# Kernel tuning notes

Measured on AMD Instinct MI355X. Metric: run time of the kernel, lower is better.

The kernel has to match this reference:

```python
import jax, jax.numpy as jnp
import numpy as np

B, S, H, I, E, K = 2, 2048, 1024, 2816, 8, 2


def setup_inputs() -> dict:
    key = jax.random.key(0)
    k1, k2, k3, k4, k5 = jax.random.split(key, 5)
    std = 0.02
    x = jax.random.normal(k1, (B, S, H), dtype=jnp.float32)
    gate_w = jax.random.normal(k2, (H, E), dtype=jnp.float32) * std   # router Linear(H,E), no bias
    Wg = jax.random.normal(k3, (E, H, I), dtype=jnp.float32) * std    # per-expert gate_proj
    Wu = jax.random.normal(k4, (E, H, I), dtype=jnp.float32) * std    # per-expert up_proj
    Wd = jax.random.normal(k5, (E, I, H), dtype=jnp.float32) * std    # per-expert down_proj
    return {"x": x, "gate_w": gate_w, "Wg": Wg, "Wu": Wu, "Wd": Wd}


def reference(x, gate_w, Wg, Wu, Wd):
    b, s, h = x.shape
    e = gate_w.shape[1]
    # --- Gating ---
    logits = jnp.einsum('bsh,he->bse', x, gate_w)                      # [B,S,E]
    top_vals, top_idx = jax.lax.top_k(logits, K)                       # [B,S,K]
    sel = (top_idx[..., None] == jnp.arange(e)).any(axis=-2)           # [B,S,E] bool, top-k mask
    sparse_logits = jnp.where(sel, logits, -jnp.inf)
    sparse_probs = jax.nn.softmax(sparse_logits, axis=-1)              # zero weight off top-k
    # --- Experts (dense over E, weighted by sparse probs; math identical to gather/scatter loop) ---
    xf = x.reshape(-1, h)                                              # [T,H], T=B*S
    g = jnp.einsum('th,ehi->tei', xf, Wg)                              # [T,E,I]
    u = jnp.einsum('th,ehi->tei', xf, Wu)
    act = jax.nn.silu(g) * u                                           # SwiGLU
    expert_out = jnp.einsum('tei,eih->teh', act, Wd)                   # [T,E,H]
    out = jnp.einsum('teh,te->th', expert_out, sparse_probs.reshape(-1, e))
    final_outputs = out.reshape(b, s, h)
    gate_logit = logits.reshape(-1, e)                                 # [B*S,E]
    return final_outputs, gate_logit
```

## Files before the change

kernel.cpp:

```cpp
#include <hip/hip_runtime.h>


namespace {
constexpr int TOKS = 4096;
constexpr int HDIM = 1024;
constexpr int IDIM = 2816;
constexpr int NEXP = 8;
constexpr int NROW = 8192;

constexpr size_t WGT_OFF = 0;
constexpr size_t WUT_OFF = 46137344;
constexpr size_t WDT_OFF = 92274688;
constexpr size_t A_OFF   = 138412032;
constexpr size_t ACT_OFF = 155189248;
constexpr size_t CNT_OFF = 201326592;
constexpr size_t OFS_OFF = CNT_OFF + 64;
constexpr size_t TLN_OFF = CNT_OFF + 128;
constexpr size_t TLS_OFF = CNT_OFF + 256;
constexpr size_t TIX_OFF = CNT_OFF + 1024;
constexpr size_t TPR_OFF = CNT_OFF + 66560;
constexpr size_t PRT_OFF = 0;
}

typedef __attribute__((ext_vector_type(8))) short short8;
typedef __attribute__((ext_vector_type(8))) unsigned short ushort8;
typedef __attribute__((ext_vector_type(4))) float f32x4;

__device__ __forceinline__ unsigned short f2bf(float f) {
  union { float f; unsigned int u; } v; v.f = f;
  unsigned int u = v.u;
  return (unsigned short)((u + 0x7fffu + ((u >> 16) & 1u)) >> 16);
}

__device__ __forceinline__ void gl2lds16(const void* g, void* l) {
  __builtin_amdgcn_global_load_lds(
      (const __attribute__((address_space(1))) void*)g,
      (__attribute__((address_space(3))) void*)l, 16, 0, 0);
}

__global__ __launch_bounds__(256) void k_transpose_all(
    const float* __restrict__ Wg, const float* __restrict__ Wu,
    const float* __restrict__ Wd, unsigned short* __restrict__ WgT,
    unsigned short* __restrict__ WuT, unsigned short* __restrict__ WdT,
    int* __restrict__ cnt) {
  const int z = blockIdx.z;
  if (z == 0 && blockIdx.x == 0 && threadIdx.x < NEXP) cnt[threadIdx.x] = 0;
  const float* in; unsigned short* out; int C, R;
  if (z < 8)       { in = Wg; out = WgT; C = IDIM; R = HDIM; }
  else if (z < 16) { in = Wu; out = WuT; C = IDIM; R = HDIM; }
  else             { in = Wd; out = WdT; C = HDIM; R = IDIM; }
  const size_t eoff = (size_t)(z & 7) * HDIM * IDIM;
  in += eoff; out += eoff;
  const int nbx = C / 64;
  const int c0 = (blockIdx.x % nbx) * 64, r0 = (blockIdx.x / nbx) * 64;
  __shared__ float tile[64][65];
  const int tid = threadIdx.x;
  const int rr = tid >> 4, cc4 = (tid & 15) * 4;
#pragma unroll
  for (int i = 0; i < 4; ++i) {
    int r = rr + i * 16;
    float4 v = *(const float4*)(in + (size_t)(r0 + r) * C + c0 + cc4);
    tile[r][cc4 + 0] = v.x; tile[r][cc4 + 1] = v.y;
    tile[r][cc4 + 2] = v.z; tile[r][cc4 + 3] = v.w;
  }
  __syncthreads();
  const int j = tid & 7;
#pragma unroll
  for (int i = 0; i < 2; ++i) {
    int c = (tid >> 3) + i * 32;
    ushort8 o;
#pragma unroll
    for (int k = 0; k < 8; ++k) o[k] = f2bf(tile[j * 8 + k][c]);
    *(ushort8*)(out + (size_t)(c0 + c) * R + r0 + j * 8) = o;
  }
}

__global__ __launch_bounds__(256) void k_gating(
    const float* __restrict__ x, const float* __restrict__ gw,
    float* __restrict__ logits_out, int* __restrict__ cnt,
    int4* __restrict__ tidx, float2* __restrict__ tprb) {
  const int lane = threadIdx.x & 63;
  const int t = blockIdx.x * 4 + (threadIdx.x >> 6);
  const float4* xr = (const float4*)(x + (size_t)t * HDIM);
  double acc[8];
#pragma unroll
  for (int e = 0; e < 8; ++e) acc[e] = 0.0;
#pragma unroll
  for (int jj = 0; jj < 4; ++jj) {
    float4 xv = xr[lane + jj * 64];
    const int hb = (lane + jj * 64) * 4;
    const float xs[4] = {xv.x, xv.y, xv.z, xv.w};
#pragma unroll
    for (int c = 0; c < 4; ++c) {
      const float4* g = (const float4*)(gw + (size_t)(hb + c) * 8);
      float4 g0 = g[0], g1 = g[1];
      acc[0] += (double)xs[c] * g0.x; acc[1] += (double)xs[c] * g0.y;
      acc[2] += (double)xs[c] * g0.z; acc[3] += (double)xs[c] * g0.w;
      acc[4] += (double)xs[c] * g1.x; acc[5] += (double)xs[c] * g1.y;
      acc[6] += (double)xs[c] * g1.z; acc[7] += (double)xs[c] * g1.w;
    }
  }
#pragma unroll
  for (int off = 32; off > 0; off >>= 1) {
#pragma unroll
    for (int e = 0; e < 8; ++e) acc[e] += __shfl_down(acc[e], off);
  }
  if (lane == 0) {
    float lg[8];
#pragma unroll
    for (int e = 0; e < 8; ++e) lg[e] = (float)acc[e];
#pragma unroll
    for (int e = 0; e < 8; ++e) logits_out[(size_t)t * 8 + e] = lg[e];
    float v0 = lg[0]; int i0 = 0; float v1 = -3.0e38f; int i1 = 0;
#pragma unroll
    for (int e = 1; e < 8; ++e) {
      if (lg[e] > v0) { v1 = v0; i1 = i0; v0 = lg[e]; i0 = e; }
      else if (lg[e] > v1) { v1 = lg[e]; i1 = e; }
    }
    float ex = expf(v1 - v0);
    float p0 = 1.0f / (1.0f + ex);
    float p1 = ex / (1.0f + ex);
    int r0 = atomicAdd(&cnt[i0], 1);
    int r1 = atomicAdd(&cnt[i1], 1);
    tidx[t] = make_int4(i0, i1, r0, r1);
    tprb[t] = make_float2(p0, p1);
  }
}

__global__ void k_prefix(const int* __restrict__ cnt, int* __restrict__ offs,
                         int2* __restrict__ tlist, int* __restrict__ tln) {
  if (threadIdx.x == 0) {
    int s = 0, nt = 0;
    for (int e = 0; e < NEXP; ++e) {
      offs[e] = s;
      for (int m0 = 0; m0 < cnt[e]; m0 += 128) tlist[nt++] = make_int2(e, m0);
      s += cnt[e];
    }
    *tln = nt;
  }
}

__global__ __launch_bounds__(256) void k_build(
    const float* __restrict__ x, const int4* __restrict__ tidx,
    const int* __restrict__ offs, unsigned short* __restrict__ A) {
  const int t = blockIdx.x;
  const int4 ii = tidx[t];
  const int r0 = offs[ii.x] + ii.z, r1 = offs[ii.y] + ii.w;
  float4 v = ((const float4*)(x + (size_t)t * HDIM))[threadIdx.x];
  ushort4 b;
  b.x = f2bf(v.x); b.y = f2bf(v.y); b.z = f2bf(v.z); b.w = f2bf(v.w);
  ((ushort4*)(A + (size_t)r0 * HDIM))[threadIdx.x] = b;
  ((ushort4*)(A + (size_t)r1 * HDIM))[threadIdx.x] = b;
}

__global__ __launch_bounds__(256, 2) void k_gemm1(
    const unsigned short* __restrict__ A, const unsigned short* __restrict__ WgT,
    const unsigned short* __restrict__ WuT, unsigned short* __restrict__ act,
    const int* __restrict__ cnt, const int* __restrict__ offs,
    const int2* __restrict__ tlist, const int* __restrict__ tln) {
  if ((int)blockIdx.y >= *tln) return;
  const int2 tl = tlist[blockIdx.y];
  const int e = tl.x, m0 = tl.y;
  const int ne = cnt[e];
  const int off = offs[e];
  const int n0 = blockIdx.x * 64;
  const unsigned short* Bg = WgT + ((size_t)e * IDIM + n0) * HDIM;
  const unsigned short* Bu = WuT + ((size_t)e * IDIM + n0) * HDIM;

  __shared__ unsigned short As[128 * 64];
  __shared__ unsigned short Bgs[64 * 64];
  __shared__ unsigned short Bus[64 * 64];

  const int tid = threadIdx.x, w = tid >> 6, lane = tid & 63;
  const int lrow8 = lane >> 3;
  const int swz = ((lane & 7) ^ lrow8) * 8;
  const int m16 = lane & 15, quad = lane >> 4, l7 = lane & 7;

  f32x4 accg[2][4], accu[2][4];
#pragma unroll
  for (int mi = 0; mi < 2; ++mi)
#pragma unroll
    for (int ni = 0; ni < 4; ++ni) {
      accg[mi][ni] = (f32x4){0.f, 0.f, 0.f, 0.f};
      accu[mi][ni] = (f32x4){0.f, 0.f, 0.f, 0.f};
    }

  for (int kt = 0; kt < HDIM / 64; ++kt) {
    const int k0 = kt * 64;
#pragma unroll
    for (int i = 0; i < 4; ++i) {
      int gr = off + m0 + w * 32 + i * 8 + lrow8;
      gr = gr > (NROW - 1) ? (NROW - 1) : gr;
      gl2lds16(A + (size_t)gr * HDIM + k0 + swz, &As[(w * 32 + i * 8) * 64]);
    }
#pragma unroll
    for (int i = 0; i < 2; ++i) {
      int rl = w * 16 + i * 8 + lrow8;
      gl2lds16(Bg + (size_t)rl * HDIM + k0 + swz, &Bgs[(w * 16 + i * 8) * 64]);
      gl2lds16(Bu + (size_t)rl * HDIM + k0 + swz, &Bus[(w * 16 + i * 8) * 64]);
    }
    __syncthreads();
#pragma unroll
    for (int kk = 0; kk < 2; ++kk) {
      const int jc = ((kk * 4 + quad) ^ l7) * 8;
      short8 af[2], bgf[4], buf[4];
#pragma unroll
      for (int mi = 0; mi < 2; ++mi)
        af[mi] = *(const short8*)&As[(w * 32 + mi * 16 + m16) * 64 + jc];
#pragma unroll
      for (int ni = 0; ni < 4; ++ni) {
        bgf[ni] = *(const short8*)&Bgs[(ni * 16 + m16) * 64 + jc];
        buf[ni] = *(const short8*)&Bus[(ni * 16 + m16) * 64 + jc];
      }
#pragma unroll
      for (int mi = 0; mi < 2; ++mi)
#pragma unroll
        for (int ni = 0; ni < 4; ++ni) {
          accg[mi][ni] = __builtin_amdgcn_mfma_f32_16x16x32_bf16(
              af[mi], bgf[ni], accg[mi][ni], 0, 0, 0);
          accu[mi][ni] = __builtin_amdgcn_mfma_f32_16x16x32_bf16(
              af[mi], buf[ni], accu[mi][ni], 0, 0, 0);
        }
    }
    __syncthreads();
  }
#pragma unroll
  for (int mi = 0; mi < 2; ++mi)
#pragma unroll
    for (int ni = 0; ni < 4; ++ni)
#pragma unroll
      for (int r = 0; r < 4; ++r) {
        int ml = w * 32 + mi * 16 + quad * 4 + r;
        float g = accg[mi][ni][r];
        float u = accu[mi][ni][r];
        float s = g / (1.0f + __expf(-g));
        As[ml * 64 + ni * 16 + m16] = f2bf(s * u);
      }
  __syncthreads();
#pragma unroll
  for (int i = 0; i < 4; ++i) {
    int chunk = i * 256 + tid;
    int row = chunk >> 3, j = chunk & 7;
    if (m0 + row < ne)
      *(ushort8*)&act[(size_t)(off + m0 + row) * IDIM + n0 + j * 8] =
          *(const ushort8*)&As[row * 64 + j * 8];
  }
}

__global__ __launch_bounds__(256, 2) void k_gemm2(
    const unsigned short* __restrict__ act, const unsigned short* __restrict__ WdT,
    float* __restrict__ partial, const int* __restrict__ cnt,
    const int* __restrict__ offs, const int2* __restrict__ tlist,
    const int* __restrict__ tln) {
  if ((int)blockIdx.y >= *tln) return;
  const int2 tl = tlist[blockIdx.y];
  const int e = tl.x, m0 = tl.y;
  const int ne = cnt[e];
  const int off = offs[e];
  const int n0 = blockIdx.x * 128;
  const unsigned short* B = WdT + ((size_t)e * HDIM + n0) * IDIM;

  __shared__ unsigned short As[128 * 64];
  __shared__ unsigned short Bs[128 * 64];

  const int tid = threadIdx.x, w = tid >> 6, lane = tid & 63;
  const int lrow8 = lane >> 3;
  const int swz = ((lane & 7) ^ lrow8) * 8;
  const int m16 = lane & 15, quad = lane >> 4, l7 = lane & 7;
  const int wm = (w >> 1) * 64, wn = (w & 1) * 64;

  f32x4 acc[4][4];
#pragma unroll
  for (int mi = 0; mi < 4; ++mi)
#pragma unroll
    for (int ni = 0; ni < 4; ++ni) acc[mi][ni] = (f32x4){0.f, 0.f, 0.f, 0.f};

  for (int kt = 0; kt < IDIM / 64; ++kt) {
    const int k0 = kt * 64;
#pragma unroll
    for (int i = 0; i < 4; ++i) {
      int rl = w * 32 + i * 8 + lrow8;
      int gr = off + m0 + rl;
      gr = gr > (NROW - 1) ? (NROW - 1) : gr;
      gl2lds16(act + (size_t)gr * IDIM + k0 + swz, &As[(w * 32 + i * 8) * 64]);
      gl2lds16(B + (size_t)rl * IDIM + k0 + swz, &Bs[(w * 32 + i * 8) * 64]);
    }
    __syncthreads();
#pragma unroll
    for (int kk = 0; kk < 2; ++kk) {
      const int jc = ((kk * 4 + quad) ^ l7) * 8;
      short8 af[4], bf[4];
#pragma unroll
      for (int mi = 0; mi < 4; ++mi)
        af[mi] = *(const short8*)&As[(wm + mi * 16 + m16) * 64 + jc];
#pragma unroll
      for (int ni = 0; ni < 4; ++ni)
        bf[ni] = *(const short8*)&Bs[(wn + ni * 16 + m16) * 64 + jc];
#pragma unroll
      for (int mi = 0; mi < 4; ++mi)
#pragma unroll
        for (int ni = 0; ni < 4; ++ni)
          acc[mi][ni] = __builtin_amdgcn_mfma_f32_16x16x32_bf16(
              af[mi], bf[ni], acc[mi][ni], 0, 0, 0);
    }
    __syncthreads();
  }
#pragma unroll
  for (int mi = 0; mi < 4; ++mi)
#pragma unroll
    for (int ni = 0; ni < 4; ++ni)
#pragma unroll
      for (int r = 0; r < 4; ++r) {
        int ml = wm + mi * 16 + quad * 4 + r;
        if (m0 + ml < ne)
          partial[(size_t)(off + m0 + ml) * HDIM + n0 + wn + ni * 16 + m16] =
              acc[mi][ni][r];
      }
}

__global__ __launch_bounds__(256) void k_combine(
    const float* __restrict__ partial, const int4* __restrict__ tidx,
    const int* __restrict__ offs, const float2* __restrict__ tprb,
    float* __restrict__ out) {
  const int t = blockIdx.x;
  const int4 ii = tidx[t];
  const int r0 = offs[ii.x] + ii.z, r1 = offs[ii.y] + ii.w;
  const float2 p = tprb[t];
  float4 a = ((const float4*)(partial + (size_t)r0 * HDIM))[threadIdx.x];
  float4 b = ((const float4*)(partial + (size_t)r1 * HDIM))[threadIdx.x];
  float4 o;
  o.x = p.x * a.x + p.y * b.x;
  o.y = p.x * a.y + p.y * b.y;
  o.z = p.x * a.z + p.y * b.z;
  o.w = p.x * a.w + p.y * b.w;
  ((float4*)(out + (size_t)t * HDIM))[threadIdx.x] = o;
}

extern "C" void kernel_launch(void* const* d_in, const int* in_sizes, int n_in,
                              void* d_out, int out_size, void* d_ws, size_t ws_size,
                              hipStream_t stream) {
  const float* x  = (const float*)d_in[0];
  const float* gw = (const float*)d_in[1];
  const float* Wg = (const float*)d_in[2];
  const float* Wu = (const float*)d_in[3];
  const float* Wd = (const float*)d_in[4];
  float* out = (float*)d_out;
  char* ws = (char*)d_ws;

  unsigned short* WgT = (unsigned short*)(ws + WGT_OFF);
  unsigned short* WuT = (unsigned short*)(ws + WUT_OFF);
  unsigned short* WdT = (unsigned short*)(ws + WDT_OFF);
  unsigned short* A   = (unsigned short*)(ws + A_OFF);
  unsigned short* act = (unsigned short*)(ws + ACT_OFF);
  float* partial = (float*)(ws + PRT_OFF);
  int* cnt  = (int*)(ws + CNT_OFF);
  int* offs = (int*)(ws + OFS_OFF);
  int* tln  = (int*)(ws + TLN_OFF);
  int2* tlist = (int2*)(ws + TLS_OFF);
  int4* tidx = (int4*)(ws + TIX_OFF);
  float2* tprb = (float2*)(ws + TPR_OFF);

  float* logits_out = out + (size_t)TOKS * HDIM;

  k_transpose_all<<<dim3(704, 1, 24), 256, 0, stream>>>(Wg, Wu, Wd, WgT, WuT,
                                                        WdT, cnt);
  k_gating<<<TOKS / 4, 256, 0, stream>>>(x, gw, logits_out, cnt, tidx, tprb);
  k_prefix<<<1, 64, 0, stream>>>(cnt, offs, tlist, tln);
  k_build<<<TOKS, 256, 0, stream>>>(x, tidx, offs, A);
  k_gemm1<<<dim3(IDIM / 64, 72), 256, 0, stream>>>(A, WgT, WuT, act, cnt, offs,
                                                   tlist, tln);
  k_gemm2<<<dim3(HDIM / 128, 72), 256, 0, stream>>>(act, WdT, partial, cnt,
                                                    offs, tlist, tln);
  k_combine<<<TOKS, 256, 0, stream>>>(partial, tidx, offs, tprb, out);
}
```

Measured before the change: 593.0 us.

## Double MoE GEMM M-tile to 256 rows and drop prefix kernel

Both expert GEMMs now process 256 routed rows per block instead of 128, with larger accumulator arrays and more A-tile loads per warp. The aim is to halve how often each expert's weight tiles are re-streamed from memory. The single-thread prefix kernel and the tile list are removed. Each GEMM block maps its blockIdx.y to an expert and row offset from the counts, and build/combine compute row offsets inline. The larger tiles raise register pressure (128 accumulator registers per thread) and leave more padded rows in each expert's last tile, which may hurt occupancy.

```diff
diff --git a/kernel.cpp b/kernel.cpp
--- a/kernel.cpp
+++ b/kernel.cpp
@@ -7,6 +7,7 @@
 constexpr int IDIM = 2816;
 constexpr int NEXP = 8;
 constexpr int NROW = 8192;
+constexpr int MTILES = 40;
 
 constexpr size_t WGT_OFF = 0;
 constexpr size_t WUT_OFF = 46137344;
@@ -14,9 +15,6 @@
 constexpr size_t A_OFF   = 138412032;
 constexpr size_t ACT_OFF = 155189248;
 constexpr size_t CNT_OFF = 201326592;
-constexpr size_t OFS_OFF = CNT_OFF + 64;
-constexpr size_t TLN_OFF = CNT_OFF + 128;
-constexpr size_t TLS_OFF = CNT_OFF + 256;
 constexpr size_t TIX_OFF = CNT_OFF + 1024;
 constexpr size_t TPR_OFF = CNT_OFF + 66560;
 constexpr size_t PRT_OFF = 0;
@@ -36,6 +34,22 @@
   __builtin_amdgcn_global_load_lds(
       (const __attribute__((address_space(1))) void*)g,
       (__attribute__((address_space(3))) void*)l, 16, 0, 0);
+}
+
+__device__ __forceinline__ void tile_map(const int* __restrict__ cnt, int y,
+                                         int& e, int& m0, int& off, int& ne) {
+  e = -1; m0 = 0; off = 0; ne = 0;
+  int s = 0;
+#pragma unroll
+  for (int ee = 0; ee < NEXP; ++ee) {
+    int c = cnt[ee];
+    int nt = (c + 255) >> 8;
+    if (e < 0) {
+      if (y < nt) { e = ee; m0 = y << 8; off = s; ne = c; }
+      else y -= nt;
+    }
+    s += c;
+  }
 }
 
 __global__ __launch_bounds__(256) void k_transpose_all(
@@ -127,25 +141,19 @@
   }
 }
 
-__global__ void k_prefix(const int* __restrict__ cnt, int* __restrict__ offs,
-                         int2* __restrict__ tlist, int* __restrict__ tln) {
-  if (threadIdx.x == 0) {
-    int s = 0, nt = 0;
-    for (int e = 0; e < NEXP; ++e) {
-      offs[e] = s;
-      for (int m0 = 0; m0 < cnt[e]; m0 += 128) tlist[nt++] = make_int2(e, m0);
-      s += cnt[e];
-    }
-    *tln = nt;
-  }
-}
-
 __global__ __launch_bounds__(256) void k_build(
     const float* __restrict__ x, const int4* __restrict__ tidx,
-    const int* __restrict__ offs, unsigned short* __restrict__ A) {
+    const int* __restrict__ cnt, unsigned short* __restrict__ A) {
   const int t = blockIdx.x;
   const int4 ii = tidx[t];
-  const int r0 = offs[ii.x] + ii.z, r1 = offs[ii.y] + ii.w;
+  int o0 = 0, o1 = 0;
+#pragma unroll
+  for (int e = 0; e < NEXP - 1; ++e) {
+    int c = cnt[e];
+    o0 += (e < ii.x) ? c : 0;
+    o1 += (e < ii.y) ? c : 0;
+  }
+  const int r0 = o0 + ii.z, r1 = o1 + ii.w;
   float4 v = ((const float4*)(x + (size_t)t * HDIM))[threadIdx.x];
   ushort4 b;
   b.x = f2bf(v.x); b.y = f2bf(v.y); b.z = f2bf(v.z); b.w = f2bf(v.w);
@@ -156,18 +164,15 @@
 __global__ __launch_bounds__(256, 2) void k_gemm1(
     const unsigned short* __restrict__ A, const unsigned short* __restrict__ WgT,
     const unsigned short* __restrict__ WuT, unsigned short* __restrict__ act,
-    const int* __restrict__ cnt, const int* __restrict__ offs,
-    const int2* __restrict__ tlist, const int* __restrict__ tln) {
-  if ((int)blockIdx.y >= *tln) return;
-  const int2 tl = tlist[blockIdx.y];
-  const int e = tl.x, m0 = tl.y;
-  const int ne = cnt[e];
-  const int off = offs[e];
+    const int* __restrict__ cnt) {
+  int e, m0, off, ne;
+  tile_map(cnt, blockIdx.y, e, m0, off, ne);
+  if (e < 0) return;
   const int n0 = blockIdx.x * 64;
   const unsigned short* Bg = WgT + ((size_t)e * IDIM + n0) * HDIM;
   const unsigned short* Bu = WuT + ((size_t)e * IDIM + n0) * HDIM;
 
-  __shared__ unsigned short As[128 * 64];
+  __shared__ unsigned short As[256 * 64];
   __shared__ unsigned short Bgs[64 * 64];
   __shared__ unsigned short Bus[64 * 64];
 
@@ -176,9 +181,9 @@
   const int swz = ((lane & 7) ^ lrow8) * 8;
   const int m16 = lane & 15, quad = lane >> 4, l7 = lane & 7;
 
-  f32x4 accg[2][4], accu[2][4];
-#pragma unroll
-  for (int mi = 0; mi < 2; ++mi)
+  f32x4 accg[4][4], accu[4][4];
+#pragma unroll
+  for (int mi = 0; mi < 4; ++mi)
 #pragma unroll
     for (int ni = 0; ni < 4; ++ni) {
       accg[mi][ni] = (f32x4){0.f, 0.f, 0.f, 0.f};
@@ -188,10 +193,10 @@
   for (int kt = 0; kt < HDIM / 64; ++kt) {
     const int k0 = kt * 64;
 #pragma unroll
-    for (int i = 0; i < 4; ++i) {
-      int gr = off + m0 + w * 32 + i * 8 + lrow8;
+    for (int i = 0; i < 8; ++i) {
+      int gr = off + m0 + w * 64 + i * 8 + lrow8;
       gr = gr > (NROW - 1) ? (NROW - 1) : gr;
-      gl2lds16(A + (size_t)gr * HDIM + k0 + swz, &As[(w * 32 + i * 8) * 64]);
+      gl2lds16(A + (size_t)gr * HDIM + k0 + swz, &As[(w * 64 + i * 8) * 64]);
     }
 #pragma unroll
     for (int i = 0; i < 2; ++i) {
@@ -203,17 +208,17 @@
 #pragma unroll
     for (int kk = 0; kk < 2; ++kk) {
       const int jc = ((kk * 4 + quad) ^ l7) * 8;
-      short8 af[2], bgf[4], buf[4];
-#pragma unroll
-      for (int mi = 0; mi < 2; ++mi)
-        af[mi] = *(const short8*)&As[(w * 32 + mi * 16 + m16) * 64 + jc];
+      short8 af[4], bgf[4], buf[4];
+#pragma unroll
+      for (int mi = 0; mi < 4; ++mi)
+        af[mi] = *(const short8*)&As[(w * 64 + mi * 16 + m16) * 64 + jc];
 #pragma unroll
       for (int ni = 0; ni < 4; ++ni) {
         bgf[ni] = *(const short8*)&Bgs[(ni * 16 + m16) * 64 + jc];
         buf[ni] = *(const short8*)&Bus[(ni * 16 + m16) * 64 + jc];
       }
 #pragma unroll
-      for (int mi = 0; mi < 2; ++mi)
+      for (int mi = 0; mi < 4; ++mi)
 #pragma unroll
         for (int ni = 0; ni < 4; ++ni) {
           accg[mi][ni] = __builtin_amdgcn_mfma_f32_16x16x32_bf16(
@@ -225,12 +230,12 @@
     __syncthreads();
   }
 #pragma unroll
-  for (int mi = 0; mi < 2; ++mi)
+  for (int mi = 0; mi < 4; ++mi)
 #pragma unroll
     for (int ni = 0; ni < 4; ++ni)
 #pragma unroll
       for (int r = 0; r < 4; ++r) {
-        int ml = w * 32 + mi * 16 + quad * 4 + r;
+        int ml = w * 64 + mi * 16 + quad * 4 + r;
         float g = accg[mi][ni][r];
         float u = accu[mi][ni][r];
         float s = g / (1.0f + __expf(-g));
@@ -238,7 +243,7 @@
       }
   __syncthreads();
 #pragma unroll
-  for (int i = 0; i < 4; ++i) {
+  for (int i = 0; i < 8; ++i) {
     int chunk = i * 256 + tid;
     int row = chunk >> 3, j = chunk & 7;
     if (m0 + row < ne)
@@ -249,55 +254,59 @@
 
 __global__ __launch_bounds__(256, 2) void k_gemm2(
     const unsigned short* __restrict__ act, const unsigned short* __restrict__ WdT,
-    float* __restrict__ partial, const int* __restrict__ cnt,
-    const int* __restrict__ offs, const int2* __restrict__ tlist,
-    const int* __restrict__ tln) {
-  if ((int)blockIdx.y >= *tln) return;
-  const int2 tl = tlist[blockIdx.y];
-  const int e = tl.x, m0 = tl.y;
-  const int ne = cnt[e];
-  const int off = offs[e];
+    float* __restrict__ partial, const int* __restrict__ cnt) {
+  int e, m0, off, ne;
+  tile_map(cnt, blockIdx.y, e, m0, off, ne);
+  if (e < 0) return;
   const int n0 = blockIdx.x * 128;
   const unsigned short* B = WdT + ((size_t)e * HDIM + n0) * IDIM;
 
-  __shared__ unsigned short As[128 * 64];
+  __shared__ unsigned short As[256 * 64];
   __shared__ unsigned short Bs[128 * 64];
 
   const int tid = threadIdx.x, w = tid >> 6, lane = tid & 63;
   const int lrow8 = lane >> 3;
   const int swz = ((lane & 7) ^ lrow8) * 8;
   const int m16 = lane & 15, quad = lane >> 4, l7 = lane & 7;
-  const int wm = (w >> 1) * 64, wn = (w & 1) * 64;
-
-  f32x4 acc[4][4];
-#pragma unroll
-  for (int mi = 0; mi < 4; ++mi)
+  const int wm = (w >> 1) * 128, wn = (w & 1) * 64;
+
+  f32x4 acc[8][4];
+#pragma unroll
+  for (int mi = 0; mi < 8; ++mi)
 #pragma unroll
     for (int ni = 0; ni < 4; ++ni) acc[mi][ni] = (f32x4){0.f, 0.f, 0.f, 0.f};
 
   for (int kt = 0; kt < IDIM / 64; ++kt) {
     const int k0 = kt * 64;
 #pragma unroll
-    for (int i = 0; i < 4; ++i) {
+    for (int i = 0; i < 8; ++i) {
+      int gr = off + m0 + w * 64 + i * 8 + lrow8;
+      gr = gr > (NROW - 1) ? (NROW - 1) : gr;
+      gl2lds16(act + (size_t)gr * IDIM + k0 + swz, &As[(w * 64 + i * 8) * 64]);
+    }
+#pragma unroll
+    for (int i = 0; i < 2; ++i) {
       int rl = w * 32 + i * 8 + lrow8;
-      int gr = off + m0 + rl;
-      gr = gr > (NROW - 1) ? (NROW - 1) : gr;
-      gl2lds16(act + (size_t)gr * IDIM + k0 + swz, &As[(w * 32 + i * 8) * 64]);
       gl2lds16(B + (size_t)rl * IDIM + k0 + swz, &Bs[(w * 32 + i * 8) * 64]);
+    }
+#pragma unroll
+    for (int i = 2; i < 4; ++i) {
+      int rl = w * 32 + (i - 2) * 8 + lrow8 + 16;
+      gl2lds16(B + (size_t)rl * IDIM + k0 + swz, &Bs[(w * 32 + 16 + (i - 2) * 8) * 64]);
     }
     __syncthreads();
 #pragma unroll
     for (int kk = 0; kk < 2; ++kk) {
       const int jc = ((kk * 4 + quad) ^ l7) * 8;
-      short8 af[4], bf[4];
-#pragma unroll
-      for (int mi = 0; mi < 4; ++mi)
+      short8 af[8], bf[4];
+#pragma unroll
+      for (int mi = 0; mi < 8; ++mi)
         af[mi] = *(const short8*)&As[(wm + mi * 16 + m16) * 64 + jc];
 #pragma unroll
       for (int ni = 0; ni < 4; ++ni)
         bf[ni] = *(const short8*)&Bs[(wn + ni * 16 + m16) * 64 + jc];
 #pragma unroll
-      for (int mi = 0; mi < 4; ++mi)
+      for (int mi = 0; mi < 8; ++mi)
 #pragma unroll
         for (int ni = 0; ni < 4; ++ni)
           acc[mi][ni] = __builtin_amdgcn_mfma_f32_16x16x32_bf16(
@@ -306,7 +315,7 @@
     __syncthreads();
   }
 #pragma unroll
-  for (int mi = 0; mi < 4; ++mi)
+  for (int mi = 0; mi < 8; ++mi)
 #pragma unroll
     for (int ni = 0; ni < 4; ++ni)
 #pragma unroll
@@ -320,11 +329,18 @@
 
 __global__ __launch_bounds__(256) void k_combine(
     const float* __restrict__ partial, const int4* __restrict__ tidx,
-    const int* __restrict__ offs, const float2* __restrict__ tprb,
+    const int* __restrict__ cnt, const float2* __restrict__ tprb,
     float* __restrict__ out) {
   const int t = blockIdx.x;
   const int4 ii = tidx[t];
-  const int r0 = offs[ii.x] + ii.z, r1 = offs[ii.y] + ii.w;
+  int o0 = 0, o1 = 0;
+#pragma unroll
+  for (int e = 0; e < NEXP - 1; ++e) {
+    int c = cnt[e];
+    o0 += (e < ii.x) ? c : 0;
+    o1 += (e < ii.y) ? c : 0;
+  }
+  const int r0 = o0 + ii.z, r1 = o1 + ii.w;
   const float2 p = tprb[t];
   float4 a = ((const float4*)(partial + (size_t)r0 * HDIM))[threadIdx.x];
   float4 b = ((const float4*)(partial + (size_t)r1 * HDIM))[threadIdx.x];
@@ -354,9 +370,6 @@
   unsigned short* act = (unsigned short*)(ws + ACT_OFF);
   float* partial = (float*)(ws + PRT_OFF);
   int* cnt  = (int*)(ws + CNT_OFF);
-  int* offs = (int*)(ws + OFS_OFF);
-  int* tln  = (int*)(ws + TLN_OFF);
-  int2* tlist = (int2*)(ws + TLS_OFF);
   int4* tidx = (int4*)(ws + TIX_OFF);
   float2* tprb = (float2*)(ws + TPR_OFF);
 
@@ -365,11 +378,8 @@
   k_transpose_all<<<dim3(704, 1, 24), 256, 0, stream>>>(Wg, Wu, Wd, WgT, WuT,
                                                         WdT, cnt);
   k_gating<<<TOKS / 4, 256, 0, stream>>>(x, gw, logits_out, cnt, tidx, tprb);
-  k_prefix<<<1, 64, 0, stream>>>(cnt, offs, tlist, tln);
-  k_build<<<TOKS, 256, 0, stream>>>(x, tidx, offs, A);
-  k_gemm1<<<dim3(IDIM / 64, 72), 256, 0, stream>>>(A, WgT, WuT, act, cnt, offs,
-                                                   tlist, tln);
-  k_gemm2<<<dim3(HDIM / 128, 72), 256, 0, stream>>>(act, WdT, partial, cnt,
-                                                    offs, tlist, tln);
-  k_combine<<<TOKS, 256, 0, stream>>>(partial, tidx, offs, tprb, out);
-}
+  k_build<<<TOKS, 256, 0, stream>>>(x, tidx, cnt, A);
+  k_gemm1<<<dim3(IDIM / 64, MTILES), 256, 0, stream>>>(A, WgT, WuT, act, cnt);
+  k_gemm2<<<dim3(HDIM / 128, MTILES), 256, 0, stream>>>(act, WdT, partial, cnt);
+  k_combine<<<TOKS, 256, 0, stream>>>(partial, tidx, cnt, tprb, out);
+}
```

After: 609.9 us. 2.8% more time.
